# Kernel optimization log

Hardware: AMD Instinct MI355X
Metric: run time of the kernel (lower is better)

Reference implementation:

```python
import jax, jax.numpy as jnp
import numpy as np

N = 100000
E = 1600000
IN_F = 256
OUT_F = 128
ALPHA = 0.2  # LeakyReLU negative slope


def setup_inputs() -> dict:
    key = jax.random.key(0)
    k_x, k_e, k_w, k_al, k_ar = jax.random.split(key, 5)
    x = jax.random.normal(k_x, (N, IN_F), dtype=jnp.float32)
    edge_index = jax.random.randint(k_e, (2, E), 0, N, dtype=jnp.int64)
    # xavier_uniform with gain=1.414
    gain = 1.414
    lim_w = gain * np.sqrt(6.0 / (IN_F + OUT_F))
    W = jax.random.uniform(k_w, (IN_F, OUT_F), dtype=jnp.float32, minval=-lim_w, maxval=lim_w)
    lim_a = gain * np.sqrt(6.0 / (OUT_F + 1))
    a_left = jax.random.uniform(k_al, (OUT_F, 1), dtype=jnp.float32, minval=-lim_a, maxval=lim_a)
    a_right = jax.random.uniform(k_ar, (OUT_F, 1), dtype=jnp.float32, minval=-lim_a, maxval=lim_a)
    return {"x": x, "edge_index": edge_index, "W": W, "a_left": a_left, "a_right": a_right}


def reference(x, edge_index, W, a_left, a_right):
    src = edge_index[0]  # destination of aggregation (rows of adj)
    dst = edge_index[1]  # neighbor being attended to
    Wh = x @ W                              # [N, out_f]
    e_left = (Wh @ a_left)[:, 0]            # [N]
    e_right = (Wh @ a_right)[:, 0]          # [N]
    e = e_left[src] + e_right[dst]          # [E]
    e = jnp.where(e > 0, e, ALPHA * e)      # LeakyReLU
    # segment softmax over edges grouped by src node
    e_max = jax.ops.segment_max(e, src, num_segments=N)          # [N]
    e_exp = jnp.exp(e - e_max[src])                               # [E]
    e_sum = jax.ops.segment_sum(e_exp, src, num_segments=N)       # [N]
    alpha = e_exp / (e_sum[src] + 1e-9)                           # [E]
    messages = alpha[:, None] * Wh[dst]                           # [E, out_f]
    output = jax.ops.segment_sum(messages, src, num_segments=N)   # [N, out_f]
    return jax.nn.relu(output)
```

## Files before the change

### kernel.cpp

```cpp
#include <hip/hip_runtime.h>
#include <cstdint>
#include <cstddef>

static constexpr int IN_F  = 256;
static constexpr int OUT_F = 128;
#define ALPHA_SLOPE 0.2f
#define NB 256
#define BUCK_SH 7
#define CAP 6144

typedef __attribute__((ext_vector_type(8))) short short8;
typedef __attribute__((ext_vector_type(4))) float f32x4;
union ABFrag { uint32_t u[4]; short8 v; };

#define AS1 __attribute__((address_space(1)))
#define AS3 __attribute__((address_space(3)))

__device__ __forceinline__ uint32_t pack_bf2(float lo, float hi) {
    uint32_t ul = __float_as_uint(lo), uh = __float_as_uint(hi);
    uint32_t rl = (ul + 0x7fffu + ((ul >> 16) & 1u)) >> 16;
    uint32_t rh = (uh + 0x7fffu + ((uh >> 16) & 1u)) & 0xffff0000u;
    return rl | rh;
}
__device__ __forceinline__ uint32_t cvtpk_bf2(float lo, float hi) {
    uint32_t r;
    asm("v_cvt_pk_bf16_f32 %0, %1, %2" : "=v"(r) : "v"(lo), "v"(hi));
    return r;
}
__device__ __forceinline__ float blo(uint32_t w) { return __uint_as_float(w << 16); }
__device__ __forceinline__ float bhi(uint32_t w) { return __uint_as_float(w & 0xffff0000u); }

__device__ __forceinline__ int edge_at(const void* ei, int idx, int is64) {
    return is64 ? (int)((const long long*)ei)[idx] : ((const int*)ei)[idx];
}

__global__ __launch_bounds__(256) void prep_hist_kernel(
    const float* __restrict__ W, const float* __restrict__ aL,
    const float* __restrict__ aR, const void* __restrict__ EI,
    int E, int nbuk, uint32_t* __restrict__ WtH,
    float* __restrict__ waL, float* __restrict__ waR, int* __restrict__ C)
{
    if (blockIdx.x < 64) {
        int dd = blockIdx.x * 256 + threadIdx.x;
        int n  = dd >> 7;
        int kd = (dd & 127) ^ ((n & 7) << 2);
        int k  = kd * 2;
        WtH[dd] = pack_bf2(W[(size_t)k * OUT_F + n], W[(size_t)(k + 1) * OUT_F + n]);
        return;
    }
    if (blockIdx.x == 64) {
        int k = threadIdx.x;
        const float* wr = W + (size_t)k * OUT_F;
        float sl = 0.f, sr = 0.f;
        for (int j = 0; j < OUT_F; j++) {
            float wv = wr[j];
            sl = fmaf(wv, aL[j], sl);
            sr = fmaf(wv, aR[j], sr);
        }
        waL[k] = sl; waR[k] = sr;
        return;
    }
    __shared__ int h[800];
    __shared__ int det;
    if (threadIdx.x == 0) det = 0;
    for (int b = threadIdx.x; b < nbuk; b += 256) h[b] = 0;
    __syncthreads();
    {
        const unsigned* eu = (const unsigned*)EI;
        int nz = 0;
        for (int i = threadIdx.x; i < 1024; i += 256)
            if (eu[2 * i + 1] != 0u) nz++;
        if (nz) atomicAdd(&det, 1);
    }
    __syncthreads();
    const int is64 = (det == 0);
    const int bid = blockIdx.x - 65;
    int chunk = (E + NB - 1) / NB;
    int start = bid * chunk;
    int end = min(start + chunk, E);
    for (int i = start + threadIdx.x; i < end; i += 256) {
        int s = edge_at(EI, i, is64);
        atomicAdd(&h[s >> BUCK_SH], 1);
    }
    __syncthreads();
    for (int b = threadIdx.x; b < nbuk; b += 256)
        C[b * NB + bid] = h[b];
}

__global__ __launch_bounds__(256) void scan1_kernel(const int* __restrict__ counts,
                                                    int* __restrict__ offsets,
                                                    int* __restrict__ partials, int N) {
    __shared__ int wt[4];
    int gid = blockIdx.x * 256 + threadIdx.x;
    const int lane = threadIdx.x & 63, wave = threadIdx.x >> 6;
    int c = (gid < N) ? counts[gid] : 0;
    int incl = c;
#pragma unroll
    for (int o = 1; o < 64; o <<= 1) {
        int v = __shfl_up(incl, o);
        if (lane >= o) incl += v;
    }
    if (lane == 63) wt[wave] = incl;
    __syncthreads();
    int woff = 0;
    for (int w = 0; w < wave; w++) woff += wt[w];
    if (gid < N) offsets[gid] = woff + incl - c;
    if (threadIdx.x == 0) partials[blockIdx.x] = wt[0] + wt[1] + wt[2] + wt[3];
}

__global__ __launch_bounds__(256) void scan2_kernel(int* data, int n) {
    __shared__ int wt[4];
    __shared__ int carry_s;
    if (threadIdx.x == 0) carry_s = 0;
    __syncthreads();
    const int lane = threadIdx.x & 63, wave = threadIdx.x >> 6;
    for (int base = 0; base < n; base += 256) {
        int i = base + threadIdx.x;
        int c = (i < n) ? data[i] : 0;
        int incl = c;
#pragma unroll
        for (int o = 1; o < 64; o <<= 1) {
            int v = __shfl_up(incl, o);
            if (lane >= o) incl += v;
        }
        if (lane == 63) wt[wave] = incl;
        __syncthreads();
        int woff = 0;
        for (int w = 0; w < wave; w++) woff += wt[w];
        int total = wt[0] + wt[1] + wt[2] + wt[3];
        int carry = carry_s;
        __syncthreads();
        if (i < n) data[i] = carry + woff + incl - c;
        if (threadIdx.x == 0) carry_s = carry + total;
        __syncthreads();
    }
}

__global__ __launch_bounds__(512, 4) void gemm_scatter_kernel(
    const float* __restrict__ X, const uint32_t* __restrict__ WtH,
    const float* __restrict__ waL, const float* __restrict__ waR,
    uint32_t* __restrict__ Whh, float* __restrict__ el, float* __restrict__ er,
    int M, const void* __restrict__ EI, int E, int nbuk,
    const int* __restrict__ Cx, const int* __restrict__ T,
    uint32_t* __restrict__ entries, int GB)
{
    __shared__ uint32_t ldsW[16384];
    __shared__ float    ldsWA[512];
    __shared__ int cur[800];
    __shared__ int det;
    const int tid = threadIdx.x;

    if (blockIdx.x >= GB) {
        if (tid == 0) det = 0;
        for (int b = tid; b < nbuk; b += 512) cur[b] = 0;
        __syncthreads();
        {
            const unsigned* eu = (const unsigned*)EI;
            int nz = 0;
            for (int i = tid; i < 1024; i += 512)
                if (eu[2 * i + 1] != 0u) nz++;
            if (nz) atomicAdd(&det, 1);
        }
        __syncthreads();
        const int is64 = (det == 0);
        const int bid = blockIdx.x - GB;
        int chunk = (E + NB - 1) / NB;
        int start = bid * chunk;
        int end = min(start + chunk, E);
        for (int i = start + tid; i < end; i += 512) {
            int s = edge_at(EI, i, is64);
            int d = edge_at(EI, E + i, is64);
            int b = s >> BUCK_SH;
            int pos = T[b] + Cx[b * NB + bid] + atomicAdd(&cur[b], 1);
            entries[pos] = ((uint32_t)(s & 127) << 17) | (uint32_t)d;
        }
        return;
    }

    const int w = tid >> 6, l = tid & 63;
    const int c = l & 15, kg = l >> 4;
    const int swz = (c & 7) << 2;

    const int bm = blockIdx.x * 128;
    const int myrow = w * 16 + c;
    const int grow = min(bm + myrow, M - 1);
    const bool rv = (bm + myrow) < M;
    const float* xp = X + (size_t)grow * IN_F + kg * 8;

    {
        const float* wsrc = (tid < 256) ? (waL + tid) : (waR + (tid - 256));
        __builtin_amdgcn_global_load_lds((AS1 const void*)wsrc,
                                         (AS3 void*)&ldsWA[tid], 4, 0, 0);
    }
    {
        const uint4* wsrc = (const uint4*)WtH;
        uint4* wdst = (uint4*)ldsW;
#pragma unroll
        for (int i = 0; i < 8; i++)
            __builtin_amdgcn_global_load_lds((AS1 const void*)(wsrc + tid + i * 512),
                                             (AS3 void*)(wdst + tid + i * 512), 16, 0, 0);
    }
    __builtin_amdgcn_sched_barrier(0);

    f32x4 xv[16];
#define GLOAD(DST, OFFS) \
    asm volatile("global_load_dwordx4 %0, %1, off offset:" OFFS : "=v"(DST) : "v"(xp))
    GLOAD(xv[0],  "0");   GLOAD(xv[1],  "16");
    GLOAD(xv[2],  "128"); GLOAD(xv[3],  "144");
    GLOAD(xv[4],  "256"); GLOAD(xv[5],  "272");
    GLOAD(xv[6],  "384"); GLOAD(xv[7],  "400");
    GLOAD(xv[8],  "512"); GLOAD(xv[9],  "528");
    GLOAD(xv[10], "640"); GLOAD(xv[11], "656");
    GLOAD(xv[12], "768"); GLOAD(xv[13], "784");
    GLOAD(xv[14], "896"); GLOAD(xv[15], "912");
#undef GLOAD
    __builtin_amdgcn_sched_barrier(0);

    f32x4 acc[8];
#pragma unroll
    for (int j = 0; j < 8; j++) acc[j] = (f32x4){0.f, 0.f, 0.f, 0.f};
    float sl = 0.f, sr = 0.f;

    asm volatile("s_waitcnt vmcnt(16)");
    __builtin_amdgcn_sched_barrier(0);
    __builtin_amdgcn_s_barrier();
    __builtin_amdgcn_sched_barrier(0);

#define GSTEP(KS, VMS)                                                        \
    {                                                                         \
        asm volatile("s_waitcnt vmcnt(" VMS ")");                             \
        __builtin_amdgcn_sched_barrier(0);                                    \
        f32x4 xa = xv[2 * KS], xb = xv[2 * KS + 1];                           \
        f32x4 l0 = *(const f32x4*)&ldsWA[KS * 32 + kg * 8];                   \
        f32x4 l1 = *(const f32x4*)&ldsWA[KS * 32 + kg * 8 + 4];               \
        f32x4 r0 = *(const f32x4*)&ldsWA[256 + KS * 32 + kg * 8];             \
        f32x4 r1 = *(const f32x4*)&ldsWA[256 + KS * 32 + kg * 8 + 4];         \
        _Pragma("unroll")                                                     \
        for (int i = 0; i < 4; i++) {                                         \
            sl = fmaf(xa[i], l0[i], sl); sl = fmaf(xb[i], l1[i], sl);         \
            sr = fmaf(xa[i], r0[i], sr); sr = fmaf(xb[i], r1[i], sr);         \
        }                                                                     \
        ABFrag a;                                                             \
        a.u[0] = cvtpk_bf2(xa[0], xa[1]); a.u[1] = cvtpk_bf2(xa[2], xa[3]);   \
        a.u[2] = cvtpk_bf2(xb[0], xb[1]); a.u[3] = cvtpk_bf2(xb[2], xb[3]);   \
        const int kd = KS * 16 + kg * 4;                                      \
        _Pragma("unroll")                                                     \
        for (int j = 0; j < 8; j++) {                                         \
            const int col = j * 16 + c;                                       \
            ABFrag b;                                                         \
            *(uint4*)b.u = *(const uint4*)&ldsW[col * 128 + (kd ^ swz)];      \
            acc[j] = __builtin_amdgcn_mfma_f32_16x16x32_bf16(a.v, b.v, acc[j], 0, 0, 0); \
        }                                                                     \
    }
    GSTEP(0, "14"); GSTEP(1, "12"); GSTEP(2, "10"); GSTEP(3, "8");
    GSTEP(4, "6");  GSTEP(5, "4");  GSTEP(6, "2");  GSTEP(7, "0");
#undef GSTEP

    sl += __shfl_xor(sl, 16); sl += __shfl_xor(sl, 32);
    sr += __shfl_xor(sr, 16); sr += __shfl_xor(sr, 32);
    if (rv && kg == 0) { el[bm + myrow] = sl; er[bm + myrow] = sr; }

    __syncthreads();
    float* sc = (float*)ldsW + w * 2048;
#pragma unroll
    for (int j = 0; j < 8; j++)
#pragma unroll
        for (int r = 0; r < 4; r++)
            sc[(kg * 4 + r) * 128 + j * 16 + c] = acc[j][r];
    __syncthreads();
#pragma unroll
    for (int m = 0; m < 16; m++) {
        float2 p = *(const float2*)&sc[m * 128 + 2 * l];
        int orow = bm + w * 16 + m;
        if (orow < M) Whh[(size_t)orow * 64 + l] = cvtpk_bf2(p.x, p.y);
    }
}

__global__ __launch_bounds__(256) void bucket_node_kernel(
    const uint32_t* __restrict__ entries, const int* __restrict__ T,
    const float* __restrict__ el, const float* __restrict__ er,
    const uint32_t* __restrict__ WhH, float* __restrict__ out,
    int E, int N, int nbuk)
{
    __shared__ int outD[CAP];
    __shared__ int cnt[128], pre[128], cur[128];
    __shared__ int wt4[1];
    const int b = blockIdx.x;
    const int tid = threadIdx.x;
    const int base = T[b];
    const int cend = (b + 1 < nbuk) ? T[b + 1] : E;
    int count = cend - base;
    if (count > CAP) count = CAP;

    if (tid < 128) { cnt[tid] = 0; cur[tid] = 0; }
    __syncthreads();
    for (int k = tid; k < count; k += 256)
        atomicAdd(&cnt[entries[base + k] >> 17], 1);
    __syncthreads();
    {
        const int lane = tid & 63, w = tid >> 6;
        int c = (tid < 128) ? cnt[tid] : 0;
        int incl = c;
#pragma unroll
        for (int o = 1; o < 64; o <<= 1) {
            int v = __shfl_up(incl, o);
            if (lane >= o) incl += v;
        }
        if (w == 0 && lane == 63) wt4[0] = incl;
        __syncthreads();
        if (tid < 128) pre[tid] = ((w == 1) ? wt4[0] : 0) + incl - c;
        __syncthreads();
    }
    for (int k = tid; k < count; k += 256) {
        uint32_t e = entries[base + k];
        int sl = e >> 17;
        int p = pre[sl] + atomicAdd(&cur[sl], 1);
        outD[p] = (int)(e & 0x1FFFFu);
    }
    __syncthreads();

    const int node0 = b << BUCK_SH;
    const int nnode = min(128, N - node0);
    const int lane = tid & 63;
    const int g = lane >> 4, q = lane & 15;

    for (int nd = (tid >> 6); nd < nnode; nd += 4) {
        const int node = node0 + nd;
        const int s0 = pre[nd];
        const int deg = cnt[nd];
        const float eli = el[node];

        if (deg <= 64) {
            int dj = 0;
            float e = -3.402823466e38f;
            if (lane < deg) {
                dj = outD[s0 + lane];
                float t = eli + er[dj];
                e = t > 0.f ? t : ALPHA_SLOPE * t;
            }
            float m = e;
#pragma unroll
            for (int o = 32; o > 0; o >>= 1) m = fmaxf(m, __shfl_xor(m, o));
            float ex = (lane < deg) ? expf(e - m) : 0.f;
            float ssum = ex;
#pragma unroll
            for (int o = 32; o > 0; o >>= 1) ssum += __shfl_xor(ssum, o);
            float p = ex / (ssum + 1e-9f);

            float a0 = 0.f, a1 = 0.f, a2 = 0.f, a3 = 0.f;
            float a4 = 0.f, a5 = 0.f, a6 = 0.f, a7 = 0.f;
            int rounds = (deg + 3) >> 2;
            int r = 0;
            for (; r + 4 <= rounds; r += 4) {
                int i0 = (r << 2) + g, i1 = i0 + 4, i2 = i0 + 8, i3 = i0 + 12;
                float p0 = __shfl(p, i0), p1 = __shfl(p, i1);
                float p2 = __shfl(p, i2), p3 = __shfl(p, i3);
                int   e0 = __shfl(dj, i0), e1 = __shfl(dj, i1);
                int   e2 = __shfl(dj, i2), e3 = __shfl(dj, i3);
                uint4 w0 = *(const uint4*)&WhH[(size_t)e0 * 64 + q * 4];
                uint4 w1 = *(const uint4*)&WhH[(size_t)e1 * 64 + q * 4];
                uint4 w2 = *(const uint4*)&WhH[(size_t)e2 * 64 + q * 4];
                uint4 w3 = *(const uint4*)&WhH[(size_t)e3 * 64 + q * 4];
                a0 = fmaf(p0, blo(w0.x), a0); a1 = fmaf(p0, bhi(w0.x), a1);
                a2 = fmaf(p0, blo(w0.y), a2); a3 = fmaf(p0, bhi(w0.y), a3);
                a4 = fmaf(p0, blo(w0.z), a4); a5 = fmaf(p0, bhi(w0.z), a5);
                a6 = fmaf(p0, blo(w0.w), a6); a7 = fmaf(p0, bhi(w0.w), a7);
                a0 = fmaf(p1, blo(w1.x), a0); a1 = fmaf(p1, bhi(w1.x), a1);
                a2 = fmaf(p1, blo(w1.y), a2); a3 = fmaf(p1, bhi(w1.y), a3);
                a4 = fmaf(p1, blo(w1.z), a4); a5 = fmaf(p1, bhi(w1.z), a5);
                a6 = fmaf(p1, blo(w1.w), a6); a7 = fmaf(p1, bhi(w1.w), a7);
                a0 = fmaf(p2, blo(w2.x), a0); a1 = fmaf(p2, bhi(w2.x), a1);
                a2 = fmaf(p2, blo(w2.y), a2); a3 = fmaf(p2, bhi(w2.y), a3);
                a4 = fmaf(p2, blo(w2.z), a4); a5 = fmaf(p2, bhi(w2.z), a5);
                a6 = fmaf(p2, blo(w2.w), a6); a7 = fmaf(p2, bhi(w2.w), a7);
                a0 = fmaf(p3, blo(w3.x), a0); a1 = fmaf(p3, bhi(w3.x), a1);
                a2 = fmaf(p3, blo(w3.y), a2); a3 = fmaf(p3, bhi(w3.y), a3);
                a4 = fmaf(p3, blo(w3.z), a4); a5 = fmaf(p3, bhi(w3.z), a5);
                a6 = fmaf(p3, blo(w3.w), a6); a7 = fmaf(p3, bhi(w3.w), a7);
            }
            for (; r + 2 <= rounds; r += 2) {
                int i0 = (r << 2) + g, i1 = i0 + 4;
                float p0 = __shfl(p, i0), p1 = __shfl(p, i1);
                int   e0 = __shfl(dj, i0), e1 = __shfl(dj, i1);
                uint4 w0 = *(const uint4*)&WhH[(size_t)e0 * 64 + q * 4];
                uint4 w1 = *(const uint4*)&WhH[(size_t)e1 * 64 + q * 4];
                a0 = fmaf(p0, blo(w0.x), a0); a1 = fmaf(p0, bhi(w0.x), a1);
                a2 = fmaf(p0, blo(w0.y), a2); a3 = fmaf(p0, bhi(w0.y), a3);
                a4 = fmaf(p0, blo(w0.z), a4); a5 = fmaf(p0, bhi(w0.z), a5);
                a6 = fmaf(p0, blo(w0.w), a6); a7 = fmaf(p0, bhi(w0.w), a7);
                a0 = fmaf(p1, blo(w1.x), a0); a1 = fmaf(p1, bhi(w1.x), a1);
                a2 = fmaf(p1, blo(w1.y), a2); a3 = fmaf(p1, bhi(w1.y), a3);
                a4 = fmaf(p1, blo(w1.z), a4); a5 = fmaf(p1, bhi(w1.z), a5);
                a6 = fmaf(p1, blo(w1.w), a6); a7 = fmaf(p1, bhi(w1.w), a7);
            }
            if (r < rounds) {
                int i0 = (r << 2) + g;
                float p0 = __shfl(p, i0);
                int   e0 = __shfl(dj, i0);
                uint4 w0 = *(const uint4*)&WhH[(size_t)e0 * 64 + q * 4];
                a0 = fmaf(p0, blo(w0.x), a0); a1 = fmaf(p0, bhi(w0.x), a1);
                a2 = fmaf(p0, blo(w0.y), a2); a3 = fmaf(p0, bhi(w0.y), a3);
                a4 = fmaf(p0, blo(w0.z), a4); a5 = fmaf(p0, bhi(w0.z), a5);
                a6 = fmaf(p0, blo(w0.w), a6); a7 = fmaf(p0, bhi(w0.w), a7);
            }
#pragma unroll
            for (int o = 16; o <= 32; o <<= 1) {
                a0 += __shfl_xor(a0, o); a1 += __shfl_xor(a1, o);
                a2 += __shfl_xor(a2, o); a3 += __shfl_xor(a3, o);
                a4 += __shfl_xor(a4, o); a5 += __shfl_xor(a5, o);
                a6 += __shfl_xor(a6, o); a7 += __shfl_xor(a7, o);
            }
            if (g == 0) {
                float4 o0 = make_float4(fmaxf(a0, 0.f), fmaxf(a1, 0.f),
                                        fmaxf(a2, 0.f), fmaxf(a3, 0.f));
                float4 o1 = make_float4(fmaxf(a4, 0.f), fmaxf(a5, 0.f),
                                        fmaxf(a6, 0.f), fmaxf(a7, 0.f));
                float* op = out + (size_t)node * OUT_F + q * 8;
                *(float4*)op = o0;
                *(float4*)(op + 4) = o1;
            }
            continue;
        }

        float m = -3.402823466e38f;
        for (int j = lane; j < deg; j += 64) {
            float e = eli + er[outD[s0 + j]];
            e = e > 0.f ? e : ALPHA_SLOPE * e;
            m = fmaxf(m, e);
        }
#pragma unroll
        for (int o = 32; o > 0; o >>= 1) m = fmaxf(m, __shfl_xor(m, o));

        float ssum = 0.f;
        for (int j = lane; j < deg; j += 64) {
            float e = eli + er[outD[s0 + j]];
            e = e > 0.f ? e : ALPHA_SLOPE * e;
            ssum += expf(e - m);
        }
#pragma unroll
        for (int o = 32; o > 0; o >>= 1) ssum += __shfl_xor(ssum, o);
        float inv = 1.f / (ssum + 1e-9f);

        float acc0 = 0.f, acc1 = 0.f;
        for (int bb = 0; bb < deg; bb += 64) {
            int j = bb + lane;
            float p = 0.f;
            int d = 0;
            if (j < deg) {
                d = outD[s0 + j];
                float e = eli + er[d];
                e = e > 0.f ? e : ALPHA_SLOPE * e;
                p = expf(e - m) * inv;
            }
            int cnt2 = min(64, deg - bb);
            for (int t = 0; t < cnt2; ++t) {
                float a = __uint_as_float(__builtin_amdgcn_readlane(__float_as_uint(p), t));
                int  dd = __builtin_amdgcn_readlane(d, t);
                uint32_t wv = WhH[(size_t)dd * 64 + lane];
                acc0 = fmaf(a, blo(wv), acc0);
                acc1 = fmaf(a, bhi(wv), acc1);
            }
        }
        out[(size_t)node * OUT_F + 2 * lane]     = fmaxf(acc0, 0.f);
        out[(size_t)node * OUT_F + 2 * lane + 1] = fmaxf(acc1, 0.f);
    }
}

extern "C" void kernel_launch(void* const* d_in, const int* in_sizes, int n_in,
                              void* d_out, int out_size, void* d_ws, size_t ws_size,
                              hipStream_t stream) {
    (void)n_in; (void)out_size; (void)ws_size;
    const float* X  = (const float*)d_in[0];
    const void*  EI = d_in[1];
    const float* W  = (const float*)d_in[2];
    const float* aL = (const float*)d_in[3];
    const float* aR = (const float*)d_in[4];
    float* out = (float*)d_out;
    const int N = in_sizes[0] / IN_F;
    const int E = in_sizes[1] / 2;
    const int nbuk = (N + 127) >> BUCK_SH;
    const int GB = (N + 127) / 128;

    char* ws = (char*)d_ws;
    float*    waL      = (float*)(ws + 256);
    float*    waR      = waL + 256;
    uint32_t* WtH      = (uint32_t*)(waR + 256);
    uint32_t* Whh      = WtH + 16384;
    float*    el       = (float*)(Whh + (size_t)N * 64);
    float*    er       = el + N;
    int*      T        = (int*)(er + N);
    int*      C        = T + 1024;
    int*      Cx       = C + (size_t)nbuk * NB;
    uint32_t* entries  = (uint32_t*)(Cx + (size_t)nbuk * NB);

    prep_hist_kernel<<<65 + NB, 256, 0, stream>>>(W, aL, aR, EI, E, nbuk,
                                                  WtH, waL, waR, C);
    scan1_kernel<<<nbuk, 256, 0, stream>>>(C, Cx, T, nbuk * NB);
    scan2_kernel<<<1, 256, 0, stream>>>(T, nbuk);
    gemm_scatter_kernel<<<GB + NB, 512, 0, stream>>>(X, WtH, waL, waR, Whh, el, er,
                                                     N, EI, E, nbuk, Cx, T,
                                                     entries, GB);
    bucket_node_kernel<<<nbuk, 256, 0, stream>>>(entries, T, el, er, Whh, out,
                                                 E, N, nbuk);
}
```

Measured before the change: 153.1 us.

## Read W fragments directly from global memory instead of staging in LDS

The GEMM part of gemm_scatter_kernel no longer copies the full 64 KB bf16 W and the attention vectors into shared memory. Each lane now loads its B fragments straight from global memory, which is expected to hit in L1/L2. Blocks shrink to 256 threads covering 64 rows, and the LDS transpose for the Wh output is replaced by a shuffle-based bf16 pair store. X loads become a simple one-step software prefetch instead of issuing all 16 loads up front. This removes per-block LDS fill and barriers and should raise occupancy, at the cost of more global/cache traffic for W and narrower, less coalesced output stores.

```diff
diff --git a/kernel.cpp b/kernel.cpp
--- a/kernel.cpp
+++ b/kernel.cpp
@@ -12,9 +12,6 @@
 typedef __attribute__((ext_vector_type(8))) short short8;
 typedef __attribute__((ext_vector_type(4))) float f32x4;
 union ABFrag { uint32_t u[4]; short8 v; };
-
-#define AS1 __attribute__((address_space(1)))
-#define AS3 __attribute__((address_space(3)))
 
 __device__ __forceinline__ uint32_t pack_bf2(float lo, float hi) {
     uint32_t ul = __float_as_uint(lo), uh = __float_as_uint(hi);
@@ -43,7 +40,7 @@
     if (blockIdx.x < 64) {
         int dd = blockIdx.x * 256 + threadIdx.x;
         int n  = dd >> 7;
-        int kd = (dd & 127) ^ ((n & 7) << 2);
+        int kd = dd & 127;
         int k  = kd * 2;
         WtH[dd] = pack_bf2(W[(size_t)k * OUT_F + n], W[(size_t)(k + 1) * OUT_F + n]);
         return;
@@ -136,7 +133,7 @@
     }
 }
 
-__global__ __launch_bounds__(512, 4) void gemm_scatter_kernel(
+__global__ __launch_bounds__(256) void gemm_scatter_kernel(
     const float* __restrict__ X, const uint32_t* __restrict__ WtH,
     const float* __restrict__ waL, const float* __restrict__ waR,
     uint32_t* __restrict__ Whh, float* __restrict__ el, float* __restrict__ er,
@@ -144,20 +141,18 @@
     const int* __restrict__ Cx, const int* __restrict__ T,
     uint32_t* __restrict__ entries, int GB)
 {
-    __shared__ uint32_t ldsW[16384];
-    __shared__ float    ldsWA[512];
     __shared__ int cur[800];
     __shared__ int det;
     const int tid = threadIdx.x;
 
     if (blockIdx.x >= GB) {
         if (tid == 0) det = 0;
-        for (int b = tid; b < nbuk; b += 512) cur[b] = 0;
+        for (int b = tid; b < nbuk; b += 256) cur[b] = 0;
         __syncthreads();
         {
             const unsigned* eu = (const unsigned*)EI;
             int nz = 0;
-            for (int i = tid; i < 1024; i += 512)
+            for (int i = tid; i < 1024; i += 256)
                 if (eu[2 * i + 1] != 0u) nz++;
             if (nz) atomicAdd(&det, 1);
         }
@@ -167,7 +162,7 @@
         int chunk = (E + NB - 1) / NB;
         int start = bid * chunk;
         int end = min(start + chunk, E);
-        for (int i = start + tid; i < end; i += 512) {
+        for (int i = start + tid; i < end; i += 256) {
             int s = edge_at(EI, i, is64);
             int d = edge_at(EI, E + i, is64);
             int b = s >> BUCK_SH;
@@ -179,101 +174,69 @@
 
     const int w = tid >> 6, l = tid & 63;
     const int c = l & 15, kg = l >> 4;
-    const int swz = (c & 7) << 2;
-
-    const int bm = blockIdx.x * 128;
-    const int myrow = w * 16 + c;
-    const int grow = min(bm + myrow, M - 1);
-    const bool rv = (bm + myrow) < M;
+    const int bm = blockIdx.x * 64;
+    const int row = bm + w * 16 + c;
+    const int grow = min(row, M - 1);
+    const bool rv = row < M;
     const float* xp = X + (size_t)grow * IN_F + kg * 8;
-
-    {
-        const float* wsrc = (tid < 256) ? (waL + tid) : (waR + (tid - 256));
-        __builtin_amdgcn_global_load_lds((AS1 const void*)wsrc,
-                                         (AS3 void*)&ldsWA[tid], 4, 0, 0);
-    }
-    {
-        const uint4* wsrc = (const uint4*)WtH;
-        uint4* wdst = (uint4*)ldsW;
-#pragma unroll
-        for (int i = 0; i < 8; i++)
-            __builtin_amdgcn_global_load_lds((AS1 const void*)(wsrc + tid + i * 512),
-                                             (AS3 void*)(wdst + tid + i * 512), 16, 0, 0);
-    }
-    __builtin_amdgcn_sched_barrier(0);
-
-    f32x4 xv[16];
-#define GLOAD(DST, OFFS) \
-    asm volatile("global_load_dwordx4 %0, %1, off offset:" OFFS : "=v"(DST) : "v"(xp))
-    GLOAD(xv[0],  "0");   GLOAD(xv[1],  "16");
-    GLOAD(xv[2],  "128"); GLOAD(xv[3],  "144");
-    GLOAD(xv[4],  "256"); GLOAD(xv[5],  "272");
-    GLOAD(xv[6],  "384"); GLOAD(xv[7],  "400");
-    GLOAD(xv[8],  "512"); GLOAD(xv[9],  "528");
-    GLOAD(xv[10], "640"); GLOAD(xv[11], "656");
-    GLOAD(xv[12], "768"); GLOAD(xv[13], "784");
-    GLOAD(xv[14], "896"); GLOAD(xv[15], "912");
-#undef GLOAD
-    __builtin_amdgcn_sched_barrier(0);
+    const uint32_t* bp = WtH + (size_t)c * 128 + kg * 4;
 
     f32x4 acc[8];
 #pragma unroll
     for (int j = 0; j < 8; j++) acc[j] = (f32x4){0.f, 0.f, 0.f, 0.f};
     float sl = 0.f, sr = 0.f;
 
-    asm volatile("s_waitcnt vmcnt(16)");
-    __builtin_amdgcn_sched_barrier(0);
-    __builtin_amdgcn_s_barrier();
-    __builtin_amdgcn_sched_barrier(0);
-
-#define GSTEP(KS, VMS)                                                        \
-    {                                                                         \
-        asm volatile("s_waitcnt vmcnt(" VMS ")");                             \
-        __builtin_amdgcn_sched_barrier(0);                                    \
-        f32x4 xa = xv[2 * KS], xb = xv[2 * KS + 1];                           \
-        f32x4 l0 = *(const f32x4*)&ldsWA[KS * 32 + kg * 8];                   \
-        f32x4 l1 = *(const f32x4*)&ldsWA[KS * 32 + kg * 8 + 4];               \
-        f32x4 r0 = *(const f32x4*)&ldsWA[256 + KS * 32 + kg * 8];             \
-        f32x4 r1 = *(const f32x4*)&ldsWA[256 + KS * 32 + kg * 8 + 4];         \
-        _Pragma("unroll")                                                     \
-        for (int i = 0; i < 4; i++) {                                         \
-            sl = fmaf(xa[i], l0[i], sl); sl = fmaf(xb[i], l1[i], sl);         \
-            sr = fmaf(xa[i], r0[i], sr); sr = fmaf(xb[i], r1[i], sr);         \
-        }                                                                     \
-        ABFrag a;                                                             \
-        a.u[0] = cvtpk_bf2(xa[0], xa[1]); a.u[1] = cvtpk_bf2(xa[2], xa[3]);   \
-        a.u[2] = cvtpk_bf2(xb[0], xb[1]); a.u[3] = cvtpk_bf2(xb[2], xb[3]);   \
-        const int kd = KS * 16 + kg * 4;                                      \
-        _Pragma("unroll")                                                     \
-        for (int j = 0; j < 8; j++) {                                         \
-            const int col = j * 16 + c;                                       \
-            ABFrag b;                                                         \
-            *(uint4*)b.u = *(const uint4*)&ldsW[col * 128 + (kd ^ swz)];      \
-            acc[j] = __builtin_amdgcn_mfma_f32_16x16x32_bf16(a.v, b.v, acc[j], 0, 0, 0); \
-        }                                                                     \
-    }
-    GSTEP(0, "14"); GSTEP(1, "12"); GSTEP(2, "10"); GSTEP(3, "8");
-    GSTEP(4, "6");  GSTEP(5, "4");  GSTEP(6, "2");  GSTEP(7, "0");
-#undef GSTEP
+    float4 xa = *(const float4*)xp;
+    float4 xb = *(const float4*)(xp + 4);
+
+#pragma unroll
+    for (int ks = 0; ks < 8; ks++) {
+        float4 na = make_float4(0.f, 0.f, 0.f, 0.f), nb = na;
+        if (ks < 7) {
+            na = *(const float4*)(xp + (ks + 1) * 32);
+            nb = *(const float4*)(xp + (ks + 1) * 32 + 4);
+        }
+        const float* wlp = waL + ks * 32 + kg * 8;
+        const float* wrp = waR + ks * 32 + kg * 8;
+        float4 l0 = *(const float4*)wlp, l1 = *(const float4*)(wlp + 4);
+        float4 r0 = *(const float4*)wrp, r1 = *(const float4*)(wrp + 4);
+        sl = fmaf(xa.x, l0.x, sl); sl = fmaf(xa.y, l0.y, sl);
+        sl = fmaf(xa.z, l0.z, sl); sl = fmaf(xa.w, l0.w, sl);
+        sl = fmaf(xb.x, l1.x, sl); sl = fmaf(xb.y, l1.y, sl);
+        sl = fmaf(xb.z, l1.z, sl); sl = fmaf(xb.w, l1.w, sl);
+        sr = fmaf(xa.x, r0.x, sr); sr = fmaf(xa.y, r0.y, sr);
+        sr = fmaf(xa.z, r0.z, sr); sr = fmaf(xa.w, r0.w, sr);
+        sr = fmaf(xb.x, r1.x, sr); sr = fmaf(xb.y, r1.y, sr);
+        sr = fmaf(xb.z, r1.z, sr); sr = fmaf(xb.w, r1.w, sr);
+        ABFrag a;
+        a.u[0] = cvtpk_bf2(xa.x, xa.y); a.u[1] = cvtpk_bf2(xa.z, xa.w);
+        a.u[2] = cvtpk_bf2(xb.x, xb.y); a.u[3] = cvtpk_bf2(xb.z, xb.w);
+        const uint32_t* bks = bp + ks * 16;
+#pragma unroll
+        for (int j = 0; j < 8; j++) {
+            ABFrag b;
+            *(uint4*)b.u = *(const uint4*)(bks + j * 2048);
+            acc[j] = __builtin_amdgcn_mfma_f32_16x16x32_bf16(a.v, b.v, acc[j], 0, 0, 0);
+        }
+        xa = na; xb = nb;
+    }
 
     sl += __shfl_xor(sl, 16); sl += __shfl_xor(sl, 32);
     sr += __shfl_xor(sr, 16); sr += __shfl_xor(sr, 32);
-    if (rv && kg == 0) { el[bm + myrow] = sl; er[bm + myrow] = sr; }
-
-    __syncthreads();
-    float* sc = (float*)ldsW + w * 2048;
+    if (rv && kg == 0) { el[row] = sl; er[row] = sr; }
+
 #pragma unroll
     for (int j = 0; j < 8; j++)
 #pragma unroll
-        for (int r = 0; r < 4; r++)
-            sc[(kg * 4 + r) * 128 + j * 16 + c] = acc[j][r];
-    __syncthreads();
-#pragma unroll
-    for (int m = 0; m < 16; m++) {
-        float2 p = *(const float2*)&sc[m * 128 + 2 * l];
-        int orow = bm + w * 16 + m;
-        if (orow < M) Whh[(size_t)orow * 64 + l] = cvtpk_bf2(p.x, p.y);
-    }
+        for (int r = 0; r < 4; r++) {
+            float mine = acc[j][r];
+            float part = __shfl_xor(mine, 1);
+            if (!(c & 1)) {
+                int orow = bm + w * 16 + kg * 4 + r;
+                if (orow < M)
+                    Whh[(size_t)orow * 64 + j * 8 + (c >> 1)] = cvtpk_bf2(mine, part);
+            }
+        }
 }
 
 __global__ __launch_bounds__(256) void bucket_node_kernel(
@@ -479,7 +442,7 @@
     const int N = in_sizes[0] / IN_F;
     const int E = in_sizes[1] / 2;
     const int nbuk = (N + 127) >> BUCK_SH;
-    const int GB = (N + 127) / 128;
+    const int GB = (N + 63) / 64;
 
     char* ws = (char*)d_ws;
     float*    waL      = (float*)(ws + 256);
@@ -497,7 +460,7 @@
                                                   WtH, waL, waR, C);
     scan1_kernel<<<nbuk, 256, 0, stream>>>(C, Cx, T, nbuk * NB);
     scan2_kernel<<<1, 256, 0, stream>>>(T, nbuk);
-    gemm_scatter_kernel<<<GB + NB, 512, 0, stream>>>(X, WtH, waL, waR, Whh, el, er,
+    gemm_scatter_kernel<<<GB + NB, 256, 0, stream>>>(X, WtH, waL, waR, Whh, el, er,
                                                      N, EI, E, nbuk, Cx, T,
                                                      entries, GB);
     bucket_node_kernel<<<nbuk, 256, 0, stream>>>(entries, T, el, er, Whh, out,
```

Result: slower. 198.3 us (+29.5%).
